# Kernel tuning notes

Hardware: AMD Instinct MI355X
Metric: run time of the kernel (lower is better)

The kernel has to match this reference:

```python
import jax, jax.numpy as jnp
import numpy as np

N_STEP = 8
DILATION = 1


def setup_inputs() -> dict:
    key = jax.random.key(0)
    k1, k2 = jax.random.split(key)
    B, C, T, V = 32, 128, 64, 25
    z = jax.random.normal(k1, (B, C, T, V), dtype=jnp.float32)
    W = jax.random.normal(k2, (C, C), dtype=jnp.float32) * 0.02  # channel-mixing ode weight
    b = jnp.zeros((C,), dtype=jnp.float32)
    return {"z": z, "W": W, "b": b}


def reference(z, W, b):
    # z: (B, C, T, V). ode_func acts per-frame on (C, V): linear over channels + tanh.
    B, C, T, V = z.shape

    def ode_func(x):
        # equivalent to applying the C->C linear on the '(b t) c v' layout
        return jnp.tanh(jnp.einsum('bctv,dc->bdtv', x, W) + b[None, :, None, None])

    t_idx = jnp.arange(T)
    z_shift_lst = [z]
    z_lst = [z]
    cur = z
    for i in range(1, N_STEP + 1):
        cur = cur + ode_func(cur)                      # Euler step
        shift = i * DILATION
        # gather with index (arange(T) - shift) % T  ==  circular roll by +shift along T
        rolled = jnp.roll(cur, shift, axis=2)
        mask = (t_idx >= shift)[None, None, :, None]   # zero the first shift frames
        z_shift_lst.append(jnp.where(mask, rolled, jnp.zeros((), cur.dtype)))
        z_lst.append(cur)
    z_shift = jnp.concatenate(z_shift_lst, axis=0)     # ((n_step+1)*B, C, T, V)
    z_cls = jnp.concatenate(z_lst, axis=0)             # ((n_step+1)*B, C, T, V)
    return (z_shift, z_cls)
```

## Files before the change

kernel.cpp:

```cpp
#include <hip/hip_runtime.h>

#define CC     128
#define TT     64
#define VV     25
#define BB     32
#define PP     (TT * VV)
#define CHUNK  (BB * CC * PP)
#define NSTEP  8
#define PTILE  32
#define NPT    (PP / PTILE)

typedef __attribute__((ext_vector_type(8))) __bf16 bf16x8;
typedef __attribute__((ext_vector_type(4))) float  f32x4;

__device__ __forceinline__ float fast_tanh(float x) {
    float e = __expf(2.0f * x);
    return 1.0f - 2.0f * __builtin_amdgcn_rcpf(e + 1.0f);
}

__device__ __forceinline__ void bf16_split(float y, unsigned short& h, unsigned short& lo) {
    unsigned int bits = __float_as_uint(y);
    h = (unsigned short)(bits >> 16);
    float r = y - __uint_as_float(bits & 0xffff0000u);
    lo = (unsigned short)(__float_as_uint(r) >> 16);
}

__global__ void wsplit(const float* __restrict__ W,
                       unsigned short* __restrict__ Wh, unsigned short* __restrict__ Wl) {
    int idx = blockIdx.x * 256 + threadIdx.x;
    if (idx < CC * CC) {
        unsigned short h, lo;
        bf16_split(W[idx], h, lo);
        Wh[idx] = h;
        Wl[idx] = lo;
    }
}

__global__ __launch_bounds__(256) void euler_fused(
    const float* __restrict__ z, const unsigned short* __restrict__ Wh,
    const unsigned short* __restrict__ Wl, const float* __restrict__ bias,
    float* __restrict__ out)
{
    __shared__ float          Xs[CC][PTILE];
    __shared__ unsigned short Xbh[PTILE * CC];
    __shared__ unsigned short Xbl[PTILE * CC];

    const int b   = blockIdx.y;
    const int p0  = blockIdx.x * PTILE;
    const int tid = threadIdx.x;
    const int w   = tid >> 6;
    const int lr  = tid & 15;
    const int lh  = (tid >> 4) & 3;

    bf16x8 ah[2][4], al[2][4];
    #pragma unroll
    for (int dtl = 0; dtl < 2; ++dtl) {
        const int d = (2 * w + dtl) * 16 + lr;
        #pragma unroll
        for (int ks = 0; ks < 4; ++ks) {
            const int cb = ks * 32 + lh * 8;
            ah[dtl][ks] = *(const bf16x8*)(Wh + d * CC + cb);
            al[dtl][ks] = *(const bf16x8*)(Wl + d * CC + cb);
        }
    }

    float bv[2][4];
    #pragma unroll
    for (int dtl = 0; dtl < 2; ++dtl)
        #pragma unroll
        for (int j = 0; j < 4; ++j)
            bv[dtl][j] = bias[(2 * w + dtl) * 16 + lh * 4 + j];

    const float* zb = z + (size_t)b * CC * PP + p0;
    #pragma unroll
    for (int it = 0; it < 4; ++it) {
        int slot = it * 256 + tid;
        int c  = slot >> 3;
        int po = (slot & 7) * 4;
        float4 v = *(const float4*)(zb + (size_t)c * PP + po);
        *(float4*)&Xs[c][po] = v;
        size_t o = (size_t)(b * CC + c) * PP + p0 + po;
        *(float4*)(out + o)                     = v;
        *(float4*)(out + (size_t)9 * CHUNK + o) = v;
        float vv[4] = {v.x, v.y, v.z, v.w};
        #pragma unroll
        for (int e = 0; e < 4; ++e) {
            int p = po + e;
            unsigned short h, lo;
            bf16_split(vv[e], h, lo);
            int off = (p * 256 + c * 2) ^ ((p & 7) << 4);
            *(unsigned short*)((char*)Xbh + off) = h;
            *(unsigned short*)((char*)Xbl + off) = lo;
        }
    }

    __syncthreads();

    float st[2][2][4];
    #pragma unroll
    for (int dtl = 0; dtl < 2; ++dtl)
        #pragma unroll
        for (int ntl = 0; ntl < 2; ++ntl)
            #pragma unroll
            for (int j = 0; j < 4; ++j)
                st[dtl][ntl][j] = Xs[(2 * w + dtl) * 16 + lh * 4 + j][ntl * 16 + lr];

    const int swz = (lr & 7) << 4;

    for (int i = 1; i <= NSTEP; ++i) {
        f32x4 acc[2][2];
        #pragma unroll
        for (int a0 = 0; a0 < 2; ++a0)
            #pragma unroll
            for (int a1 = 0; a1 < 2; ++a1)
                acc[a0][a1] = (f32x4){0.0f, 0.0f, 0.0f, 0.0f};

        #pragma unroll
        for (int ks = 0; ks < 4; ++ks) {
            const int ro0 = ((lr)      * 256 + ks * 64 + lh * 16) ^ swz;
            const int ro1 = ((16 + lr) * 256 + ks * 64 + lh * 16) ^ swz;
            bf16x8 bh0 = *(const bf16x8*)((const char*)Xbh + ro0);
            bf16x8 bh1 = *(const bf16x8*)((const char*)Xbh + ro1);
            bf16x8 bl0 = *(const bf16x8*)((const char*)Xbl + ro0);
            bf16x8 bl1 = *(const bf16x8*)((const char*)Xbl + ro1);
            #pragma unroll
            for (int dtl = 0; dtl < 2; ++dtl) {
                acc[dtl][0] = __builtin_amdgcn_mfma_f32_16x16x32_bf16(ah[dtl][ks], bh0, acc[dtl][0], 0, 0, 0);
                acc[dtl][1] = __builtin_amdgcn_mfma_f32_16x16x32_bf16(ah[dtl][ks], bh1, acc[dtl][1], 0, 0, 0);
                acc[dtl][0] = __builtin_amdgcn_mfma_f32_16x16x32_bf16(al[dtl][ks], bh0, acc[dtl][0], 0, 0, 0);
                acc[dtl][1] = __builtin_amdgcn_mfma_f32_16x16x32_bf16(al[dtl][ks], bh1, acc[dtl][1], 0, 0, 0);
                acc[dtl][0] = __builtin_amdgcn_mfma_f32_16x16x32_bf16(ah[dtl][ks], bl0, acc[dtl][0], 0, 0, 0);
                acc[dtl][1] = __builtin_amdgcn_mfma_f32_16x16x32_bf16(ah[dtl][ks], bl1, acc[dtl][1], 0, 0, 0);
            }
        }

        #pragma unroll
        for (int dtl = 0; dtl < 2; ++dtl)
            #pragma unroll
            for (int ntl = 0; ntl < 2; ++ntl)
                #pragma unroll
                for (int j = 0; j < 4; ++j)
                    st[dtl][ntl][j] += fast_tanh(acc[dtl][ntl][j] + bv[dtl][j]);

        __syncthreads();

        #pragma unroll
        for (int dtl = 0; dtl < 2; ++dtl) {
            const int dbase = (2 * w + dtl) * 16 + lh * 4;
            #pragma unroll
            for (int ntl = 0; ntl < 2; ++ntl) {
                const int p = ntl * 16 + lr;
                ushort4 hv, lv;
                bf16_split(st[dtl][ntl][0], hv.x, lv.x);
                bf16_split(st[dtl][ntl][1], hv.y, lv.y);
                bf16_split(st[dtl][ntl][2], hv.z, lv.z);
                bf16_split(st[dtl][ntl][3], hv.w, lv.w);
                const int off = (p * 256 + dbase * 2) ^ ((p & 7) << 4);
                *(ushort4*)((char*)Xbh + off) = hv;
                *(ushort4*)((char*)Xbl + off) = lv;
            }
        }

        __syncthreads();

        const size_t shiftBase = (size_t)i * CHUNK;
        const size_t clsBase   = (size_t)(9 + i) * CHUNK;
        const int s = VV * i;
        #pragma unroll
        for (int dtl = 0; dtl < 2; ++dtl)
            #pragma unroll
            for (int ntl = 0; ntl < 2; ++ntl) {
                const int p = p0 + ntl * 16 + lr;
                #pragma unroll
                for (int j = 0; j < 4; ++j) {
                    const int d = (2 * w + dtl) * 16 + lh * 4 + j;
                    const size_t row = (size_t)(b * CC + d) * PP;
                    const float y = st[dtl][ntl][j];
                    out[clsBase + row + p] = y;
                    const int q = p + s;
                    if (q < PP) out[shiftBase + row + q] = y;
                    if (p < s)  out[shiftBase + row + p] = 0.0f;
                }
            }
    }
}

extern "C" void kernel_launch(void* const* d_in, const int* in_sizes, int n_in,
                              void* d_out, int out_size, void* d_ws, size_t ws_size,
                              hipStream_t stream) {
    const float* z    = (const float*)d_in[0];
    const float* W    = (const float*)d_in[1];
    const float* bias = (const float*)d_in[2];
    float* out = (float*)d_out;
    unsigned short* Wh = (unsigned short*)d_ws;
    unsigned short* Wl = Wh + CC * CC;

    hipLaunchKernelGGL(wsplit, dim3((CC * CC + 255) / 256), dim3(256), 0, stream, W, Wh, Wl);
    hipLaunchKernelGGL(euler_fused, dim3(NPT, BB), dim3(256), 0, stream, z, Wh, Wl, bias, out);
}
```

Before: 605.3 us.

## Transpose MFMA operands, double-buffer LDS state, vectorize output stores

Swaps the MFMA operand roles so each lane holds four consecutive spatial positions, which lets the cls output be written as 128-bit vector stores and the shifted output take a contiguous fast path when the tile needs no masking. Activations now alternate between two LDS buffers, so each Euler step needs one barrier instead of two. The fp32 staging tile is dropped in favour of loading the initial state straight from global memory. The swizzle gains an extra XOR bit, and launch bounds request 4 blocks per CU; LDS writes become scalar 16-bit stores, which may add LDS traffic.

```diff
diff --git a/kernel.cpp b/kernel.cpp
--- a/kernel.cpp
+++ b/kernel.cpp
@@ -25,6 +25,17 @@
     lo = (unsigned short)(__float_as_uint(r) >> 16);
 }
 
+__device__ __forceinline__ int xb_off(int p, int c) {
+    return (p * 256 + c * 2) ^ ((p & 7) << 4) ^ ((p & 8) << 3);
+}
+
+__device__ __forceinline__ void lds_barrier() {
+    asm volatile("s_waitcnt lgkmcnt(0)" ::: "memory");
+    __builtin_amdgcn_sched_barrier(0);
+    __builtin_amdgcn_s_barrier();
+    __builtin_amdgcn_sched_barrier(0);
+}
+
 __global__ void wsplit(const float* __restrict__ W,
                        unsigned short* __restrict__ Wh, unsigned short* __restrict__ Wl) {
     int idx = blockIdx.x * 256 + threadIdx.x;
@@ -36,14 +47,13 @@
     }
 }
 
-__global__ __launch_bounds__(256) void euler_fused(
+__global__ __launch_bounds__(256, 4) void euler_fused(
     const float* __restrict__ z, const unsigned short* __restrict__ Wh,
     const unsigned short* __restrict__ Wl, const float* __restrict__ bias,
     float* __restrict__ out)
 {
-    __shared__ float          Xs[CC][PTILE];
-    __shared__ unsigned short Xbh[PTILE * CC];
-    __shared__ unsigned short Xbl[PTILE * CC];
+    __shared__ unsigned short XH[2][PTILE * CC];
+    __shared__ unsigned short XL[2][PTILE * CC];
 
     const int b   = blockIdx.y;
     const int p0  = blockIdx.x * PTILE;
@@ -52,24 +62,21 @@
     const int lr  = tid & 15;
     const int lh  = (tid >> 4) & 3;
 
-    bf16x8 ah[2][4], al[2][4];
-    #pragma unroll
-    for (int dtl = 0; dtl < 2; ++dtl) {
-        const int d = (2 * w + dtl) * 16 + lr;
+    bf16x8 wh[2][4], wl[2][4];
+    #pragma unroll
+    for (int dt = 0; dt < 2; ++dt) {
+        const int d = (2 * w + dt) * 16 + lr;
         #pragma unroll
         for (int ks = 0; ks < 4; ++ks) {
             const int cb = ks * 32 + lh * 8;
-            ah[dtl][ks] = *(const bf16x8*)(Wh + d * CC + cb);
-            al[dtl][ks] = *(const bf16x8*)(Wl + d * CC + cb);
-        }
-    }
-
-    float bv[2][4];
-    #pragma unroll
-    for (int dtl = 0; dtl < 2; ++dtl)
-        #pragma unroll
-        for (int j = 0; j < 4; ++j)
-            bv[dtl][j] = bias[(2 * w + dtl) * 16 + lh * 4 + j];
+            wh[dt][ks] = *(const bf16x8*)(Wh + d * CC + cb);
+            wl[dt][ks] = *(const bf16x8*)(Wl + d * CC + cb);
+        }
+    }
+
+    float bv[2];
+    #pragma unroll
+    for (int dt = 0; dt < 2; ++dt) bv[dt] = bias[(2 * w + dt) * 16 + lr];
 
     const float* zb = z + (size_t)b * CC * PP + p0;
     #pragma unroll
@@ -78,110 +85,120 @@
         int c  = slot >> 3;
         int po = (slot & 7) * 4;
         float4 v = *(const float4*)(zb + (size_t)c * PP + po);
-        *(float4*)&Xs[c][po] = v;
         size_t o = (size_t)(b * CC + c) * PP + p0 + po;
         *(float4*)(out + o)                     = v;
         *(float4*)(out + (size_t)9 * CHUNK + o) = v;
         float vv[4] = {v.x, v.y, v.z, v.w};
         #pragma unroll
         for (int e = 0; e < 4; ++e) {
-            int p = po + e;
             unsigned short h, lo;
             bf16_split(vv[e], h, lo);
-            int off = (p * 256 + c * 2) ^ ((p & 7) << 4);
-            *(unsigned short*)((char*)Xbh + off) = h;
-            *(unsigned short*)((char*)Xbl + off) = lo;
-        }
-    }
-
-    __syncthreads();
-
-    float st[2][2][4];
-    #pragma unroll
-    for (int dtl = 0; dtl < 2; ++dtl)
-        #pragma unroll
-        for (int ntl = 0; ntl < 2; ++ntl)
-            #pragma unroll
-            for (int j = 0; j < 4; ++j)
-                st[dtl][ntl][j] = Xs[(2 * w + dtl) * 16 + lh * 4 + j][ntl * 16 + lr];
-
-    const int swz = (lr & 7) << 4;
+            int off = xb_off(po + e, c);
+            *(unsigned short*)((char*)XH[0] + off) = h;
+            *(unsigned short*)((char*)XL[0] + off) = lo;
+        }
+    }
+
+    f32x4 st[2][2];
+    #pragma unroll
+    for (int pt = 0; pt < 2; ++pt)
+        #pragma unroll
+        for (int dt = 0; dt < 2; ++dt) {
+            const int d = (2 * w + dt) * 16 + lr;
+            st[pt][dt] = *(const f32x4*)(z + (size_t)(b * CC + d) * PP + p0 + pt * 16 + lh * 4);
+        }
+
+    lds_barrier();
+
+    const int swz = ((lr & 7) << 4) ^ ((lr & 8) << 3);
 
     for (int i = 1; i <= NSTEP; ++i) {
+        const char* xh = (const char*)XH[(i - 1) & 1];
+        const char* xl = (const char*)XL[(i - 1) & 1];
+
         f32x4 acc[2][2];
         #pragma unroll
-        for (int a0 = 0; a0 < 2; ++a0)
-            #pragma unroll
-            for (int a1 = 0; a1 < 2; ++a1)
-                acc[a0][a1] = (f32x4){0.0f, 0.0f, 0.0f, 0.0f};
+        for (int pt = 0; pt < 2; ++pt)
+            #pragma unroll
+            for (int dt = 0; dt < 2; ++dt)
+                acc[pt][dt] = (f32x4){0.0f, 0.0f, 0.0f, 0.0f};
 
         #pragma unroll
         for (int ks = 0; ks < 4; ++ks) {
-            const int ro0 = ((lr)      * 256 + ks * 64 + lh * 16) ^ swz;
-            const int ro1 = ((16 + lr) * 256 + ks * 64 + lh * 16) ^ swz;
-            bf16x8 bh0 = *(const bf16x8*)((const char*)Xbh + ro0);
-            bf16x8 bh1 = *(const bf16x8*)((const char*)Xbh + ro1);
-            bf16x8 bl0 = *(const bf16x8*)((const char*)Xbl + ro0);
-            bf16x8 bl1 = *(const bf16x8*)((const char*)Xbl + ro1);
-            #pragma unroll
-            for (int dtl = 0; dtl < 2; ++dtl) {
-                acc[dtl][0] = __builtin_amdgcn_mfma_f32_16x16x32_bf16(ah[dtl][ks], bh0, acc[dtl][0], 0, 0, 0);
-                acc[dtl][1] = __builtin_amdgcn_mfma_f32_16x16x32_bf16(ah[dtl][ks], bh1, acc[dtl][1], 0, 0, 0);
-                acc[dtl][0] = __builtin_amdgcn_mfma_f32_16x16x32_bf16(al[dtl][ks], bh0, acc[dtl][0], 0, 0, 0);
-                acc[dtl][1] = __builtin_amdgcn_mfma_f32_16x16x32_bf16(al[dtl][ks], bh1, acc[dtl][1], 0, 0, 0);
-                acc[dtl][0] = __builtin_amdgcn_mfma_f32_16x16x32_bf16(ah[dtl][ks], bl0, acc[dtl][0], 0, 0, 0);
-                acc[dtl][1] = __builtin_amdgcn_mfma_f32_16x16x32_bf16(ah[dtl][ks], bl1, acc[dtl][1], 0, 0, 0);
+            const int co = ks * 64 + lh * 16;
+            const int r0 = ((lr)      * 256 + co) ^ swz;
+            const int r1 = ((16 + lr) * 256 + co) ^ swz;
+            bf16x8 a0h = *(const bf16x8*)(xh + r0);
+            bf16x8 a1h = *(const bf16x8*)(xh + r1);
+            bf16x8 a0l = *(const bf16x8*)(xl + r0);
+            bf16x8 a1l = *(const bf16x8*)(xl + r1);
+            #pragma unroll
+            for (int dt = 0; dt < 2; ++dt) {
+                acc[0][dt] = __builtin_amdgcn_mfma_f32_16x16x32_bf16(a0h, wh[dt][ks], acc[0][dt], 0, 0, 0);
+                acc[1][dt] = __builtin_amdgcn_mfma_f32_16x16x32_bf16(a1h, wh[dt][ks], acc[1][dt], 0, 0, 0);
+                acc[0][dt] = __builtin_amdgcn_mfma_f32_16x16x32_bf16(a0l, wh[dt][ks], acc[0][dt], 0, 0, 0);
+                acc[1][dt] = __builtin_amdgcn_mfma_f32_16x16x32_bf16(a1l, wh[dt][ks], acc[1][dt], 0, 0, 0);
+                acc[0][dt] = __builtin_amdgcn_mfma_f32_16x16x32_bf16(a0h, wl[dt][ks], acc[0][dt], 0, 0, 0);
+                acc[1][dt] = __builtin_amdgcn_mfma_f32_16x16x32_bf16(a1h, wl[dt][ks], acc[1][dt], 0, 0, 0);
             }
         }
 
         #pragma unroll
-        for (int dtl = 0; dtl < 2; ++dtl)
-            #pragma unroll
-            for (int ntl = 0; ntl < 2; ++ntl)
+        for (int pt = 0; pt < 2; ++pt)
+            #pragma unroll
+            for (int dt = 0; dt < 2; ++dt)
                 #pragma unroll
                 for (int j = 0; j < 4; ++j)
-                    st[dtl][ntl][j] += fast_tanh(acc[dtl][ntl][j] + bv[dtl][j]);
-
-        __syncthreads();
-
-        #pragma unroll
-        for (int dtl = 0; dtl < 2; ++dtl) {
-            const int dbase = (2 * w + dtl) * 16 + lh * 4;
-            #pragma unroll
-            for (int ntl = 0; ntl < 2; ++ntl) {
-                const int p = ntl * 16 + lr;
-                ushort4 hv, lv;
-                bf16_split(st[dtl][ntl][0], hv.x, lv.x);
-                bf16_split(st[dtl][ntl][1], hv.y, lv.y);
-                bf16_split(st[dtl][ntl][2], hv.z, lv.z);
-                bf16_split(st[dtl][ntl][3], hv.w, lv.w);
-                const int off = (p * 256 + dbase * 2) ^ ((p & 7) << 4);
-                *(ushort4*)((char*)Xbh + off) = hv;
-                *(ushort4*)((char*)Xbl + off) = lv;
-            }
-        }
-
-        __syncthreads();
+                    st[pt][dt][j] += fast_tanh(acc[pt][dt][j] + bv[dt]);
+
+        if (i < NSTEP) {
+            char* yh = (char*)XH[i & 1];
+            char* yl = (char*)XL[i & 1];
+            #pragma unroll
+            for (int pt = 0; pt < 2; ++pt)
+                #pragma unroll
+                for (int dt = 0; dt < 2; ++dt) {
+                    const int d = (2 * w + dt) * 16 + lr;
+                    #pragma unroll
+                    for (int j = 0; j < 4; ++j) {
+                        const int p = pt * 16 + lh * 4 + j;
+                        unsigned short h, lo;
+                        bf16_split(st[pt][dt][j], h, lo);
+                        const int off = xb_off(p, d);
+                        *(unsigned short*)(yh + off) = h;
+                        *(unsigned short*)(yl + off) = lo;
+                    }
+                }
+        }
 
         const size_t shiftBase = (size_t)i * CHUNK;
         const size_t clsBase   = (size_t)(9 + i) * CHUNK;
         const int s = VV * i;
-        #pragma unroll
-        for (int dtl = 0; dtl < 2; ++dtl)
-            #pragma unroll
-            for (int ntl = 0; ntl < 2; ++ntl) {
-                const int p = p0 + ntl * 16 + lr;
-                #pragma unroll
-                for (int j = 0; j < 4; ++j) {
-                    const int d = (2 * w + dtl) * 16 + lh * 4 + j;
-                    const size_t row = (size_t)(b * CC + d) * PP;
-                    const float y = st[dtl][ntl][j];
-                    out[clsBase + row + p] = y;
-                    const int q = p + s;
-                    if (q < PP) out[shiftBase + row + q] = y;
-                    if (p < s)  out[shiftBase + row + p] = 0.0f;
+        const bool fast = (p0 >= s) && (p0 + PTILE - 1 + s < PP);
+        #pragma unroll
+        for (int pt = 0; pt < 2; ++pt) {
+            const int P0 = p0 + pt * 16 + lh * 4;
+            #pragma unroll
+            for (int dt = 0; dt < 2; ++dt) {
+                const int d = (2 * w + dt) * 16 + lr;
+                const size_t row = (size_t)(b * CC + d) * PP;
+                f32x4 y = st[pt][dt];
+                *(f32x4*)(out + clsBase + row + P0) = y;
+                if (fast) {
+                    float* dst = out + shiftBase + row + P0 + s;
+                    dst[0] = y[0]; dst[1] = y[1]; dst[2] = y[2]; dst[3] = y[3];
+                } else {
+                    #pragma unroll
+                    for (int e = 0; e < 4; ++e) {
+                        const int p = P0 + e, q = p + s;
+                        if (q < PP) out[shiftBase + row + q] = y[e];
+                        if (p < s)  out[shiftBase + row + p] = 0.0f;
+                    }
                 }
             }
+        }
+
+        if (i < NSTEP) lds_barrier();
     }
 }
 
```

After: 688.9 us. +13.8%, slower.
